# Kernel optimization log

Hardware: AMD Instinct MI355X
Metric: run time of the kernel (lower is better)

## Reference

```python
import jax, jax.numpy as jnp
import numpy as np

HIDDEN, HEADS, KV_HEADS, HEAD_DIM = 2048, 32, 8, 64
B, T = 2, 2048


def setup_inputs() -> dict:
    key = jax.random.key(0)
    ks = jax.random.split(key, 5)
    x = jax.random.normal(ks[0], (B, T, HIDDEN), dtype=jnp.float32)
    # additive causal mask: 0 on/below diagonal, -1e9 above
    causal = jnp.triu(jnp.full((T, T), -1e9, dtype=jnp.float32), k=1)
    attn_mask = causal[None, None, :, :]  # [1,1,T,T]
    s = 1.0 / np.sqrt(HIDDEN)
    Wq = jax.random.normal(ks[1], (HIDDEN, HEADS * HEAD_DIM), dtype=jnp.float32) * s
    Wk = jax.random.normal(ks[2], (HIDDEN, KV_HEADS * HEAD_DIM), dtype=jnp.float32) * s
    Wv = jax.random.normal(ks[3], (HIDDEN, KV_HEADS * HEAD_DIM), dtype=jnp.float32) * s
    Wo = jax.random.normal(ks[4], (HEADS * HEAD_DIM, HIDDEN), dtype=jnp.float32) * s
    return {"x": x, "attn_mask": attn_mask, "Wq": Wq, "Wk": Wk, "Wv": Wv, "Wo": Wo}


def reference(x, attn_mask, Wq, Wk, Wv, Wo):
    Bx, Tx, _ = x.shape
    # projections -> [B, heads, T, head_dim]
    q = (x @ Wq).reshape(Bx, Tx, HEADS, HEAD_DIM).transpose(0, 2, 1, 3)
    k = (x @ Wk).reshape(Bx, Tx, KV_HEADS, HEAD_DIM).transpose(0, 2, 1, 3)
    v = (x @ Wv).reshape(Bx, Tx, KV_HEADS, HEAD_DIM).transpose(0, 2, 1, 3)
    # repeat_interleave kv heads to match query heads (GQA)
    rep = HEADS // KV_HEADS
    k = jnp.repeat(k, rep, axis=1)
    v = jnp.repeat(v, rep, axis=1)
    att = jnp.einsum("bhqd,bhkd->bhqk", q, k) / np.sqrt(HEAD_DIM).astype(np.float32)
    att = att + attn_mask
    p = jax.nn.softmax(att, axis=-1)
    y = jnp.einsum("bhqk,bhkd->bhqd", p, v)
    y = y.transpose(0, 2, 1, 3).reshape(Bx, Tx, HEADS * HEAD_DIM)
    return y @ Wo
```

## Files before the change

### kernel.cpp

```cpp
#include <hip/hip_runtime.h>
#include <hip/hip_bf16.h>
#include <cmath>

#define HIDDEN 2048
#define NHEADS 32
#define NKVH   8
#define HD     64
#define BB     2
#define TSEQ   2048
#define MROWS  (BB*TSEQ)

typedef __attribute__((ext_vector_type(8))) short bf16x8;
typedef __attribute__((ext_vector_type(4))) float f32x4;

__device__ __forceinline__ ushort f2bf(float f) {
  union { float f; unsigned u; } x; x.f = f;
  unsigned r = x.u + 0x7fffu + ((x.u >> 16) & 1u);
  return (ushort)(r >> 16);
}

__device__ __forceinline__ unsigned pack_bf2(float a, float b) {
  union { float f; unsigned u; } x, y; x.f = a; y.f = b;
  return __builtin_amdgcn_perm(y.u + 0x8000u, x.u + 0x8000u, 0x07060302);
}

__device__ __forceinline__ void async16(ushort* lds, const ushort* g) {
  __builtin_amdgcn_global_load_lds(
      (const __attribute__((address_space(1))) unsigned int*)g,
      (__attribute__((address_space(3))) unsigned int*)lds, 16, 0, 0);
}

__global__ void cvt_kernel(const float* __restrict__ in, ushort* __restrict__ out, int n4) {
  int i = blockIdx.x * blockDim.x + threadIdx.x;
  if (i < n4) {
    float4 v = ((const float4*)in)[i];
    ushort4 o;
    o.x = f2bf(v.x); o.y = f2bf(v.y); o.z = f2bf(v.z); o.w = f2bf(v.w);
    ((ushort4*)out)[i] = o;
  }
}

__global__ void tcvt_kernel(const float* __restrict__ in, ushort* __restrict__ out, int R, int C, float scale) {
  __shared__ float tile[32][33];
  int tx = threadIdx.x & 31, ty = threadIdx.x >> 5;
  int c0 = blockIdx.x * 32, r0 = blockIdx.y * 32;
#pragma unroll
  for (int i = 0; i < 4; ++i)
    tile[ty*4 + i][tx] = in[(size_t)(r0 + ty*4 + i) * C + c0 + tx];
  __syncthreads();
#pragma unroll
  for (int i = 0; i < 4; ++i)
    out[(size_t)(c0 + ty*4 + i) * R + r0 + tx] = f2bf(tile[tx][ty*4 + i] * scale);
}

template<typename OutT, int OUT_MODE>
__global__ __launch_bounds__(256) void gemm_bt(const ushort* __restrict__ A,
                                               const ushort* __restrict__ BT,
                                               OutT* __restrict__ C,
                                               int M, int N, int K) {
  __shared__ ushort sA[2][128 * 32];
  __shared__ ushort sB[2][128 * 32];
  const int tid = threadIdx.x;
  const int w = tid >> 6, l = tid & 63;
  const int wr = w >> 1, wc = w & 1;
  const int g = l >> 4, c16 = l & 15;
  const int m0 = blockIdx.y * 128, n0 = blockIdx.x * 128;

  const int sr = l >> 2;
  const int sc = (l & 3) * 8;
  const int i0 = w * 2, i1 = w * 2 + 1;
  const ushort* gA[2]; const ushort* gB[2];
  gA[0] = A  + (size_t)(m0 + i0*16 + sr) * K + sc;
  gA[1] = A  + (size_t)(m0 + i1*16 + sr) * K + sc;
  gB[0] = BT + (size_t)(n0 + i0*16 + sr) * K + sc;
  gB[1] = BT + (size_t)(n0 + i1*16 + sr) * K + sc;

  f32x4 acc[4][4] = {};

  async16(&sA[0][0] + i0*512 + l*8, gA[0]);
  async16(&sA[0][0] + i1*512 + l*8, gA[1]);
  async16(&sB[0][0] + i0*512 + l*8, gB[0]);
  async16(&sB[0][0] + i1*512 + l*8, gB[1]);
  __syncthreads();

  int cur = 0;
  for (int k0 = 0; k0 < K; k0 += 32) {
    if (k0 + 32 < K) {
      ushort* dA = &sA[cur ^ 1][0];
      ushort* dB = &sB[cur ^ 1][0];
      async16(dA + i0*512 + l*8, gA[0] + k0 + 32);
      async16(dA + i1*512 + l*8, gA[1] + k0 + 32);
      async16(dB + i0*512 + l*8, gB[0] + k0 + 32);
      async16(dB + i1*512 + l*8, gB[1] + k0 + 32);
    }
    const ushort* cA = &sA[cur][0];
    const ushort* cB = &sB[cur][0];
    bf16x8 a[4], b[4];
#pragma unroll
    for (int mi = 0; mi < 4; ++mi)
      a[mi] = *(const bf16x8*)(cA + (wr*64 + mi*16 + c16) * 32 + g * 8);
#pragma unroll
    for (int nj = 0; nj < 4; ++nj)
      b[nj] = *(const bf16x8*)(cB + (wc*64 + nj*16 + c16) * 32 + g * 8);
#pragma unroll
    for (int mi = 0; mi < 4; ++mi)
#pragma unroll
      for (int nj = 0; nj < 4; ++nj)
        acc[mi][nj] = __builtin_amdgcn_mfma_f32_16x16x32_bf16(a[mi], b[nj], acc[mi][nj], 0, 0, 0);
    __syncthreads();
    cur ^= 1;
  }

#pragma unroll
  for (int mi = 0; mi < 4; ++mi) {
#pragma unroll
    for (int nj = 0; nj < 4; ++nj) {
      int gcol = n0 + wc*64 + nj*16 + c16;
#pragma unroll
      for (int jj = 0; jj < 4; ++jj) {
        int grow = m0 + wr*64 + mi*16 + g*4 + jj;
        float v = acc[mi][nj][jj];
        size_t oidx;
        if (OUT_MODE == 0) oidx = (size_t)grow * N + gcol;
        else {
          if (gcol < 2048)      oidx = (size_t)grow * 2048 + gcol;
          else if (gcol < 2560) oidx = (size_t)8388608 + (size_t)grow * 512 + (gcol - 2048);
          else                  oidx = (size_t)10485760 + ((size_t)(grow >> 11) * 512 + (gcol - 2560)) * 2048 + (grow & 2047);
        }
        if constexpr (sizeof(OutT) == 2) C[oidx] = (OutT)f2bf(v);
        else                             C[oidx] = v;
      }
    }
  }
}

__global__ __launch_bounds__(512, 2) void attn_kernel(const ushort* __restrict__ Qb,
                                                      const ushort* __restrict__ Kb,
                                                      const ushort* __restrict__ VTb,
                                                      ushort* __restrict__ Yb) {
  __shared__ ushort sK[2][4096];
  __shared__ ushort sV[2][4096];
  __shared__ ushort sP[8][2048];
  const int tid = threadIdx.x, w = tid >> 6, l = tid & 63;
  const int g = l >> 4, c16 = l & 15;
  const int bid = blockIdx.x;
  const int kvh = bid & 7, b = (bid >> 3) & 1, raw = bid >> 4;
  const int p = (raw < 16) ? raw : 47 - raw;
  const int qt = (w >> 2) ? p : 63 - p;
  const int h = kvh * 4 + (w & 3);
  const int q0 = qt * 32;
  const int my_last = (q0 + 31) >> 6;
  const int ktmax = (2047 - 32 * p) >> 6;

  const int srow = tid >> 3;
  const int scolB = ((tid & 7) << 4) ^ ((srow & 7) << 4);
  const ushort* gK = Kb  + ((size_t)(b * TSEQ) + srow) * 512 + kvh * 64 + (scolB >> 1);
  const ushort* gV = VTb + ((size_t)(b * 512 + kvh * 64) + srow) * 2048 + (scolB >> 1);
  ushort* dK = &sK[0][0] + tid * 8;
  ushort* dV = &sV[0][0] + tid * 8;

  const ushort* Qp = Qb + ((size_t)(b * TSEQ + q0)) * 2048 + h * 64;
  char* sPw = (char*)&sP[w][0];
  const float L2E = 1.44269504f;
  const float SHIFT = 16.0f * 1.44269504f;

  bf16x8 bq[2][2];
#pragma unroll
  for (int qf = 0; qf < 2; ++qf)
#pragma unroll
    for (int dc = 0; dc < 2; ++dc)
      bq[qf][dc] = *(const bf16x8*)(Qp + (size_t)(qf*16 + c16) * 2048 + dc*32 + g*8);

  float lsum[2] = {0.f, 0.f};
  f32x4 accO[4][2] = {};

  async16(dK, gK);
  async16(dV, gV);
  __syncthreads();

  int buf = 0;
  for (int kt = 0; kt <= ktmax; ++kt) {
    if (kt < ktmax) {
      async16(dK + (buf ^ 1) * 4096, gK + (size_t)(kt + 1) * 32768);
      async16(dV + (buf ^ 1) * 4096, gV + (kt + 1) * 64);
    }
    if (kt <= my_last) {
      const char* cK = (const char*)&sK[buf][0];
      const char* cV = (const char*)&sV[buf][0];

      f32x4 s[4][2] = {};
#pragma unroll
      for (int dc = 0; dc < 2; ++dc) {
        bf16x8 aK[4];
#pragma unroll
        for (int kf = 0; kf < 4; ++kf) {
          int rk = kf*16 + c16;
          aK[kf] = *(const bf16x8*)(cK + rk*128 + ((dc*64 + g*16) ^ ((rk & 7) << 4)));
        }
        __builtin_amdgcn_s_setprio(1);
#pragma unroll
        for (int kf = 0; kf < 4; ++kf)
#pragma unroll
          for (int qf = 0; qf < 2; ++qf)
            s[kf][qf] = __builtin_amdgcn_mfma_f32_16x16x32_bf16(aK[kf], bq[qf][dc], s[kf][qf], 0, 0, 0);
        __builtin_amdgcn_s_setprio(0);
      }

      if (kt == my_last) {
#pragma unroll
        for (int kf = 0; kf < 4; ++kf)
#pragma unroll
          for (int qf = 0; qf < 2; ++qf)
#pragma unroll
            for (int j = 0; j < 4; ++j)
              if (kt*64 + kf*16 + g*4 + j > q0 + qf*16 + c16) s[kf][qf][j] = -1e30f;
      }

#pragma unroll
      for (int qf = 0; qf < 2; ++qf) {
        float tk[4];
#pragma unroll
        for (int kf = 0; kf < 4; ++kf) {
          float p0 = __builtin_amdgcn_exp2f(__builtin_fmaf(s[kf][qf][0], L2E, -SHIFT));
          float p1 = __builtin_amdgcn_exp2f(__builtin_fmaf(s[kf][qf][1], L2E, -SHIFT));
          float p2 = __builtin_amdgcn_exp2f(__builtin_fmaf(s[kf][qf][2], L2E, -SHIFT));
          float p3 = __builtin_amdgcn_exp2f(__builtin_fmaf(s[kf][qf][3], L2E, -SHIFT));
          s[kf][qf][0] = p0; s[kf][qf][1] = p1; s[kf][qf][2] = p2; s[kf][qf][3] = p3;
          tk[kf] = (p0 + p1) + (p2 + p3);
        }
        lsum[qf] += (tk[0] + tk[1]) + (tk[2] + tk[3]);
      }

#pragma unroll
      for (int qf = 0; qf < 2; ++qf) {
        int q = qf*16 + c16;
#pragma unroll
        for (int kf = 0; kf < 4; ++kf) {
          uint2 pk;
          pk.x = pack_bf2(s[kf][qf][0], s[kf][qf][1]);
          pk.y = pack_bf2(s[kf][qf][2], s[kf][qf][3]);
          int byte = (q*128 + (kf*16 + g*4)*2) ^ ((q & 7) << 4);
          *(uint2*)(sPw + byte) = pk;
        }
      }

#pragma unroll
      for (int cc = 0; cc < 2; ++cc) {
        bf16x8 bp0, bp1;
        {
          int ba = (c16*128 + cc*64 + g*16) ^ ((c16 & 7) << 4);
          bp0 = *(const bf16x8*)(sPw + ba);
          int qb2 = 16 + c16;
          int bb2 = (qb2*128 + cc*64 + g*16) ^ ((qb2 & 7) << 4);
          bp1 = *(const bf16x8*)(sPw + bb2);
        }
        bf16x8 aV[4];
#pragma unroll
        for (int df = 0; df < 4; ++df) {
          int rv = df*16 + c16;
          aV[df] = *(const bf16x8*)(cV + rv*128 + ((cc*64 + g*16) ^ ((rv & 7) << 4)));
        }
        __builtin_amdgcn_s_setprio(1);
#pragma unroll
        for (int df = 0; df < 4; ++df) {
          accO[df][0] = __builtin_amdgcn_mfma_f32_16x16x32_bf16(aV[df], bp0, accO[df][0], 0, 0, 0);
          accO[df][1] = __builtin_amdgcn_mfma_f32_16x16x32_bf16(aV[df], bp1, accO[df][1], 0, 0, 0);
        }
        __builtin_amdgcn_s_setprio(0);
      }
    }
    __syncthreads();
    buf ^= 1;
  }

#pragma unroll
  for (int qf = 0; qf < 2; ++qf) {
    float t = lsum[qf];
    t += __shfl_xor(t, 16);
    t += __shfl_xor(t, 32);
    float inv = 1.f / t;
#pragma unroll
    for (int df = 0; df < 4; ++df) {
      uint2 o;
      o.x = pack_bf2(accO[df][qf][0] * inv, accO[df][qf][1] * inv);
      o.y = pack_bf2(accO[df][qf][2] * inv, accO[df][qf][3] * inv);
      *(uint2*)(Yb + ((size_t)(b * TSEQ + q0 + qf*16 + c16)) * 2048 + h*64 + df*16 + g*4) = o;
    }
  }
}

extern "C" void kernel_launch(void* const* d_in, const int* in_sizes, int n_in,
                              void* d_out, int out_size, void* d_ws, size_t ws_size,
                              hipStream_t stream) {
  const float* x  = (const float*)d_in[0];
  const float* Wq = (const float*)d_in[2];
  const float* Wk = (const float*)d_in[3];
  const float* Wv = (const float*)d_in[4];
  const float* Wo = (const float*)d_in[5];
  float* out = (float*)d_out;
  char* ws = (char*)d_ws;
  const size_t MB = 1024 * 1024;
  ushort* xb  = (ushort*)(ws);
  ushort* WqT = (ushort*)(ws + 16*MB);
  ushort* WkT = (ushort*)(ws + 24*MB);
  ushort* WvT = (ushort*)(ws + 26*MB);
  ushort* WoT = (ushort*)(ws + 28*MB);
  ushort* Qb  = (ushort*)(ws + 36*MB);
  ushort* Kb  = (ushort*)(ws + 52*MB);
  ushort* VTb = (ushort*)(ws + 56*MB);
  ushort* Yb  = xb;

  cvt_kernel<<<8192, 256, 0, stream>>>(x, xb, 2097152);
  tcvt_kernel<<<dim3(2048/32, 2048/32), 256, 0, stream>>>(Wq, WqT, 2048, 2048, 0.125f);
  tcvt_kernel<<<dim3(512/32,  2048/32), 256, 0, stream>>>(Wk, WkT, 2048, 512, 1.0f);
  tcvt_kernel<<<dim3(512/32,  2048/32), 256, 0, stream>>>(Wv, WvT, 2048, 512, 1.0f);
  tcvt_kernel<<<dim3(2048/32, 2048/32), 256, 0, stream>>>(Wo, WoT, 2048, 2048, 1.0f);

  gemm_bt<ushort, 3><<<dim3(3072/128, 4096/128), 256, 0, stream>>>(xb, WqT, Qb, MROWS, 3072, 2048);

  attn_kernel<<<512, 512, 0, stream>>>(Qb, Kb, VTb, Yb);

  gemm_bt<float, 0><<<dim3(2048/128, 4096/128), 256, 0, stream>>>(Yb, WoT, out, MROWS, 2048, 2048);
}
```

Before: 323.3 us.

## Restructure attention into 256-thread blocks with 32-key tiles and exact causal bounds

The attention kernel now uses 4 warps per block (one query tile of 32 rows, four heads of one KV group) with 32-key K/V tiles, launching 1024 blocks instead of 512. Causal tiles now line up, so each block loops to exactly its diagonal tile, removing the paired-tile load balancing and the idle iterations. Blocks are ordered longest-first to help balance. Shared memory shrinks and the P scratch uses a padded stride instead of XOR swizzle. In exchange there is more sync and barrier overhead per unit of work and less K/V reuse per block.

```diff
diff --git a/kernel.cpp b/kernel.cpp
--- a/kernel.cpp
+++ b/kernel.cpp
@@ -134,28 +134,28 @@
   }
 }
 
-__global__ __launch_bounds__(512, 2) void attn_kernel(const ushort* __restrict__ Qb,
+__global__ __launch_bounds__(256, 2) void attn_kernel(const ushort* __restrict__ Qb,
                                                       const ushort* __restrict__ Kb,
                                                       const ushort* __restrict__ VTb,
                                                       ushort* __restrict__ Yb) {
-  __shared__ ushort sK[2][4096];
-  __shared__ ushort sV[2][4096];
-  __shared__ ushort sP[8][2048];
+  __shared__ ushort sK[2][2048];
+  __shared__ ushort sV[2][2048];
+  __shared__ ushort sP[4][1280];
   const int tid = threadIdx.x, w = tid >> 6, l = tid & 63;
   const int g = l >> 4, c16 = l & 15;
   const int bid = blockIdx.x;
-  const int kvh = bid & 7, b = (bid >> 3) & 1, raw = bid >> 4;
-  const int p = (raw < 16) ? raw : 47 - raw;
-  const int qt = (w >> 2) ? p : 63 - p;
-  const int h = kvh * 4 + (w & 3);
+  const int qt = 63 - (bid >> 4);
+  const int b = (bid >> 3) & 1, kvh = bid & 7;
+  const int h = kvh * 4 + w;
   const int q0 = qt * 32;
-  const int my_last = (q0 + 31) >> 6;
-  const int ktmax = (2047 - 32 * p) >> 6;
-
-  const int srow = tid >> 3;
-  const int scolB = ((tid & 7) << 4) ^ ((srow & 7) << 4);
-  const ushort* gK = Kb  + ((size_t)(b * TSEQ) + srow) * 512 + kvh * 64 + (scolB >> 1);
-  const ushort* gV = VTb + ((size_t)(b * 512 + kvh * 64) + srow) * 2048 + (scolB >> 1);
+  const int ktmax = qt;
+
+  const int srK = tid >> 3;
+  const int scK = ((tid & 7) << 4) ^ ((srK & 7) << 4);
+  const int srV = tid >> 2;
+  const int scV = ((tid & 3) << 4) ^ ((srV & 3) << 4);
+  const ushort* gK = Kb  + ((size_t)(b * TSEQ) + srK) * 512 + kvh * 64 + (scK >> 1);
+  const ushort* gV = VTb + ((size_t)(b * 512 + kvh * 64) + srV) * 2048 + (scV >> 1);
   ushort* dK = &sK[0][0] + tid * 8;
   ushort* dV = &sV[0][0] + tid * 8;
 
@@ -181,93 +181,83 @@
   int buf = 0;
   for (int kt = 0; kt <= ktmax; ++kt) {
     if (kt < ktmax) {
-      async16(dK + (buf ^ 1) * 4096, gK + (size_t)(kt + 1) * 32768);
-      async16(dV + (buf ^ 1) * 4096, gV + (kt + 1) * 64);
-    }
-    if (kt <= my_last) {
-      const char* cK = (const char*)&sK[buf][0];
-      const char* cV = (const char*)&sV[buf][0];
-
-      f32x4 s[4][2] = {};
-#pragma unroll
-      for (int dc = 0; dc < 2; ++dc) {
-        bf16x8 aK[4];
-#pragma unroll
-        for (int kf = 0; kf < 4; ++kf) {
-          int rk = kf*16 + c16;
-          aK[kf] = *(const bf16x8*)(cK + rk*128 + ((dc*64 + g*16) ^ ((rk & 7) << 4)));
-        }
-        __builtin_amdgcn_s_setprio(1);
-#pragma unroll
-        for (int kf = 0; kf < 4; ++kf)
-#pragma unroll
-          for (int qf = 0; qf < 2; ++qf)
-            s[kf][qf] = __builtin_amdgcn_mfma_f32_16x16x32_bf16(aK[kf], bq[qf][dc], s[kf][qf], 0, 0, 0);
-        __builtin_amdgcn_s_setprio(0);
-      }
-
-      if (kt == my_last) {
-#pragma unroll
-        for (int kf = 0; kf < 4; ++kf)
-#pragma unroll
-          for (int qf = 0; qf < 2; ++qf)
-#pragma unroll
-            for (int j = 0; j < 4; ++j)
-              if (kt*64 + kf*16 + g*4 + j > q0 + qf*16 + c16) s[kf][qf][j] = -1e30f;
-      }
-
-#pragma unroll
-      for (int qf = 0; qf < 2; ++qf) {
-        float tk[4];
-#pragma unroll
-        for (int kf = 0; kf < 4; ++kf) {
-          float p0 = __builtin_amdgcn_exp2f(__builtin_fmaf(s[kf][qf][0], L2E, -SHIFT));
-          float p1 = __builtin_amdgcn_exp2f(__builtin_fmaf(s[kf][qf][1], L2E, -SHIFT));
-          float p2 = __builtin_amdgcn_exp2f(__builtin_fmaf(s[kf][qf][2], L2E, -SHIFT));
-          float p3 = __builtin_amdgcn_exp2f(__builtin_fmaf(s[kf][qf][3], L2E, -SHIFT));
-          s[kf][qf][0] = p0; s[kf][qf][1] = p1; s[kf][qf][2] = p2; s[kf][qf][3] = p3;
-          tk[kf] = (p0 + p1) + (p2 + p3);
-        }
-        lsum[qf] += (tk[0] + tk[1]) + (tk[2] + tk[3]);
-      }
-
-#pragma unroll
-      for (int qf = 0; qf < 2; ++qf) {
-        int q = qf*16 + c16;
-#pragma unroll
-        for (int kf = 0; kf < 4; ++kf) {
-          uint2 pk;
-          pk.x = pack_bf2(s[kf][qf][0], s[kf][qf][1]);
-          pk.y = pack_bf2(s[kf][qf][2], s[kf][qf][3]);
-          int byte = (q*128 + (kf*16 + g*4)*2) ^ ((q & 7) << 4);
-          *(uint2*)(sPw + byte) = pk;
-        }
-      }
-
-#pragma unroll
-      for (int cc = 0; cc < 2; ++cc) {
-        bf16x8 bp0, bp1;
-        {
-          int ba = (c16*128 + cc*64 + g*16) ^ ((c16 & 7) << 4);
-          bp0 = *(const bf16x8*)(sPw + ba);
-          int qb2 = 16 + c16;
-          int bb2 = (qb2*128 + cc*64 + g*16) ^ ((qb2 & 7) << 4);
-          bp1 = *(const bf16x8*)(sPw + bb2);
-        }
-        bf16x8 aV[4];
-#pragma unroll
-        for (int df = 0; df < 4; ++df) {
-          int rv = df*16 + c16;
-          aV[df] = *(const bf16x8*)(cV + rv*128 + ((cc*64 + g*16) ^ ((rv & 7) << 4)));
-        }
-        __builtin_amdgcn_s_setprio(1);
-#pragma unroll
-        for (int df = 0; df < 4; ++df) {
-          accO[df][0] = __builtin_amdgcn_mfma_f32_16x16x32_bf16(aV[df], bp0, accO[df][0], 0, 0, 0);
-          accO[df][1] = __builtin_amdgcn_mfma_f32_16x16x32_bf16(aV[df], bp1, accO[df][1], 0, 0, 0);
-        }
-        __builtin_amdgcn_s_setprio(0);
-      }
+      async16(dK + (buf ^ 1) * 2048, gK + (size_t)(kt + 1) * 16384);
+      async16(dV + (buf ^ 1) * 2048, gV + (kt + 1) * 32);
+    }
+    const char* cK = (const char*)&sK[buf][0];
+    const char* cV = (const char*)&sV[buf][0];
+
+    f32x4 s[2][2] = {};
+#pragma unroll
+    for (int dc = 0; dc < 2; ++dc) {
+      bf16x8 aK[2];
+#pragma unroll
+      for (int kf = 0; kf < 2; ++kf) {
+        int rk = kf*16 + c16;
+        aK[kf] = *(const bf16x8*)(cK + rk*128 + ((dc*64 + g*16) ^ ((rk & 7) << 4)));
+      }
+      __builtin_amdgcn_s_setprio(1);
+#pragma unroll
+      for (int kf = 0; kf < 2; ++kf)
+#pragma unroll
+        for (int qf = 0; qf < 2; ++qf)
+          s[kf][qf] = __builtin_amdgcn_mfma_f32_16x16x32_bf16(aK[kf], bq[qf][dc], s[kf][qf], 0, 0, 0);
+      __builtin_amdgcn_s_setprio(0);
+    }
+
+    if (kt == ktmax) {
+#pragma unroll
+      for (int kf = 0; kf < 2; ++kf)
+#pragma unroll
+        for (int qf = 0; qf < 2; ++qf)
+#pragma unroll
+          for (int j = 0; j < 4; ++j)
+            if (kf*16 + g*4 + j > qf*16 + c16) s[kf][qf][j] = -1e30f;
+    }
+
+#pragma unroll
+    for (int qf = 0; qf < 2; ++qf) {
+      float tk[2];
+#pragma unroll
+      for (int kf = 0; kf < 2; ++kf) {
+        float p0 = __builtin_amdgcn_exp2f(__builtin_fmaf(s[kf][qf][0], L2E, -SHIFT));
+        float p1 = __builtin_amdgcn_exp2f(__builtin_fmaf(s[kf][qf][1], L2E, -SHIFT));
+        float p2 = __builtin_amdgcn_exp2f(__builtin_fmaf(s[kf][qf][2], L2E, -SHIFT));
+        float p3 = __builtin_amdgcn_exp2f(__builtin_fmaf(s[kf][qf][3], L2E, -SHIFT));
+        s[kf][qf][0] = p0; s[kf][qf][1] = p1; s[kf][qf][2] = p2; s[kf][qf][3] = p3;
+        tk[kf] = (p0 + p1) + (p2 + p3);
+      }
+      lsum[qf] += tk[0] + tk[1];
+    }
+
+#pragma unroll
+    for (int qf = 0; qf < 2; ++qf) {
+      int q = qf*16 + c16;
+#pragma unroll
+      for (int kf = 0; kf < 2; ++kf) {
+        uint2 pk;
+        pk.x = pack_bf2(s[kf][qf][0], s[kf][qf][1]);
+        pk.y = pack_bf2(s[kf][qf][2], s[kf][qf][3]);
+        *(uint2*)(sPw + q*80 + kf*32 + g*8) = pk;
+      }
+    }
+
+    {
+      bf16x8 bp0 = *(const bf16x8*)(sPw + c16*80 + g*16);
+      bf16x8 bp1 = *(const bf16x8*)(sPw + (16 + c16)*80 + g*16);
+      bf16x8 aV[4];
+#pragma unroll
+      for (int df = 0; df < 4; ++df) {
+        int rv = df*16 + c16;
+        aV[df] = *(const bf16x8*)(cV + rv*64 + ((g*16) ^ ((rv & 3) << 4)));
+      }
+      __builtin_amdgcn_s_setprio(1);
+#pragma unroll
+      for (int df = 0; df < 4; ++df) {
+        accO[df][0] = __builtin_amdgcn_mfma_f32_16x16x32_bf16(aV[df], bp0, accO[df][0], 0, 0, 0);
+        accO[df][1] = __builtin_amdgcn_mfma_f32_16x16x32_bf16(aV[df], bp1, accO[df][1], 0, 0, 0);
+      }
+      __builtin_amdgcn_s_setprio(0);
     }
     __syncthreads();
     buf ^= 1;
@@ -318,7 +308,7 @@
 
   gemm_bt<ushort, 3><<<dim3(3072/128, 4096/128), 256, 0, stream>>>(xb, WqT, Qb, MROWS, 3072, 2048);
 
-  attn_kernel<<<512, 512, 0, stream>>>(Qb, Kb, VTb, Yb);
+  attn_kernel<<<1024, 256, 0, stream>>>(Qb, Kb, VTb, Yb);
 
   gemm_bt<float, 0><<<dim3(2048/128, 4096/128), 256, 0, stream>>>(Yb, WoT, out, MROWS, 2048, 2048);
 }
```

New measurement: 311.2 us. -3.8%, faster.
